# Kernel tuning notes

Measured on AMD Instinct MI355X. Metric: run time of the kernel, lower is better.

## Reference

```python
import jax, jax.numpy as jnp
import numpy as np

B, T, D, H = 4, 2048, 1024, 16
DK = D // H  # 64


def setup_inputs() -> dict:
    key = jax.random.key(0)
    ks = jax.random.split(key, 8)
    std = 1.0 / np.sqrt(2.0 * D)  # initialize_weights: normal(0, 1/sqrt(2*d_model*(i_layer+1))), i_layer=0
    inp = {
        "q": jax.random.normal(ks[0], (B, T, D), jnp.float32),
        "k": jax.random.normal(ks[1], (B, T, D), jnp.float32),
        "v": jax.random.normal(ks[2], (B, T, D), jnp.float32),
        "Wq": jax.random.normal(ks[3], (D, D), jnp.float32) * std,
        "Wk": jax.random.normal(ks[4], (D, D), jnp.float32) * std,
        "Wv": jax.random.normal(ks[5], (D, D), jnp.float32) * std,
        "Wo": jax.random.normal(ks[6], (D, D), jnp.float32) * std,
        "bq": jnp.zeros((D,), jnp.float32),
        "bk": jnp.zeros((D,), jnp.float32),
        "bv": jnp.zeros((D,), jnp.float32),
        "bo": jnp.zeros((D,), jnp.float32),
    }
    return inp


def _split_heads(x):
    # (B,T,D) -> (B,H,T,DK), same as x.view(B,T,H,DK).transpose(1,2)
    b, t, _ = x.shape
    return x.reshape(b, t, H, DK).transpose(0, 2, 1, 3)


def reference(q, k, v, Wq, Wk, Wv, Wo, bq, bk, bv, bo):
    # Linear projections (torch Linear: x @ W.T + b)
    qh = _split_heads(q @ Wq.T + bq)  # (B,H,T,DK)
    kh = _split_heads(k @ Wk.T + bk)
    vh = _split_heads(v @ Wv.T + bv)

    # scaled dot-product similarities: (B,H,Tq,Tk)
    scores = jnp.einsum("bhqd,bhkd->bhqk", qh, kh) / jnp.sqrt(jnp.float32(DK))

    # causal mask: tril(ones)==0 positions filled with -inf
    tq, tk = scores.shape[-2], scores.shape[-1]
    causal = jnp.tril(jnp.ones((tq, tk), dtype=bool))
    scores = jnp.where(causal, scores, jnp.float32(-jnp.inf))

    attn = jax.nn.softmax(scores, axis=-1)  # (B,H,Tq,Tk)
    ctx = jnp.einsum("bhqk,bhkd->bhqd", attn, vh)  # (B,H,Tq,DK)

    # merge heads: (B,H,T,DK) -> (B,T,D), then output projection
    merged = ctx.transpose(0, 2, 1, 3).reshape(q.shape[0], tq, D)
    return merged @ Wo.T + bo
```

## Files before the change

### kernel.cpp

```cpp
#include <hip/hip_runtime.h>
#include <hip/hip_bf16.h>
#include <stdint.h>

#define B_ 4
#define T_ 2048
#define D_ 1024
#define H_ 16
#define DK_ 64
#define M_ (B_*T_)

typedef __attribute__((ext_vector_type(8))) short bf16x8;
typedef __attribute__((ext_vector_type(4))) short bf16x4;
typedef __attribute__((ext_vector_type(4))) float f32x4;
typedef __hip_bfloat16 bf16;

__device__ __forceinline__ void gld_lds16(const bf16* g, bf16* l) {
  __builtin_amdgcn_global_load_lds((const __attribute__((address_space(1))) void*)g,
                                   (__attribute__((address_space(3))) void*)l,
                                   16, 0, 0);
}

__device__ __forceinline__ short bfbits(float f) {
  union { bf16 h; short s; } u; u.h = __float2bfloat16(f); return u.s;
}

__global__ __launch_bounds__(256) void cvt_all(
    const float* __restrict__ q, const float* __restrict__ k, const float* __restrict__ v,
    const float* __restrict__ wq, const float* __restrict__ wk,
    const float* __restrict__ wv, const float* __restrict__ wo,
    bf16* __restrict__ qb, bf16* __restrict__ kb, bf16* __restrict__ vb,
    bf16* __restrict__ wqb, bf16* __restrict__ wkb,
    bf16* __restrict__ wvb, bf16* __restrict__ wob) {
  int gid = blockIdx.x * 256 + threadIdx.x;
  const float* src; bf16* dst; int off;
  if (gid < 6291456) {
    int s = gid >> 21; off = gid & 2097151;
    src = (s == 0) ? q : (s == 1) ? k : v;
    dst = (s == 0) ? qb : (s == 1) ? kb : vb;
  } else {
    int g2 = gid - 6291456;
    int s = g2 >> 18; off = g2 & 262143;
    src = (s == 0) ? wq : (s == 1) ? wk : (s == 2) ? wv : wo;
    dst = (s == 0) ? wqb : (s == 1) ? wkb : (s == 2) ? wvb : wob;
  }
  float4 val = reinterpret_cast<const float4*>(src)[off];
  union { ushort4 u; bf16 h[4]; } o;
  o.h[0] = __float2bfloat16(val.x);
  o.h[1] = __float2bfloat16(val.y);
  o.h[2] = __float2bfloat16(val.z);
  o.h[3] = __float2bfloat16(val.w);
  reinterpret_cast<ushort4*>(dst)[off] = o.u;
}

__global__ __launch_bounds__(512) void proj_qkv(
    const bf16* __restrict__ qb, const bf16* __restrict__ kb, const bf16* __restrict__ vb,
    const bf16* __restrict__ Wqb, const bf16* __restrict__ Wkb, const bf16* __restrict__ Wvb,
    const float* __restrict__ bq, const float* __restrict__ bk, const float* __restrict__ bv,
    bf16* __restrict__ Qh, bf16* __restrict__ Kh, bf16* __restrict__ Vt) {
  constexpr int K = 1024;
  constexpr int BK = 64;
  __shared__ __align__(16) bf16 As[256 * BK];
  __shared__ __align__(16) bf16 Bs[128 * BK];

  const int z = blockIdx.z;
  const bool vt = (z == 2);
  const bf16* A  = (z == 0) ? qb : (z == 1) ? kb : Wvb;
  const bf16* Bm = (z == 0) ? Wqb : (z == 1) ? Wkb : vb;
  const float* bias = (z == 0) ? bq : (z == 1) ? bk : bv;
  bf16* out = (z == 0) ? Qh : (z == 1) ? Kh : Vt;
  const float scale = (z == 0) ? 0.125f * 1.4426950408889634f : 1.0f;

  const int bid = blockIdx.x + 32 * blockIdx.y;
  int bm, bn;
  if (vt) {
    bm = bid >> 6; bn = bid & 63;
  } else {
    const int xcd = bid & 7, loc = bid >> 3;
    bm = xcd * 4 + (loc & 3);
    bn = loc >> 2;
  }

  const int tid = threadIdx.x;
  const int w = tid >> 6, l = tid & 63;
  const int wm = w >> 1, wn = w & 1;
  const int lr = l & 15, lk = l >> 4;

  f32x4 acc[4][4] = {};

  for (int k0 = 0; k0 < K; k0 += BK) {
#pragma unroll
    for (int i = 0; i < 4; ++i) {
      int p = i * 512 + tid;
      int row = p >> 3;
      int so = (p & 7) ^ (row & 7);
      gld_lds16(A + (size_t)(bm * 256 + row) * K + k0 + so * 8, &As[p * 8]);
    }
#pragma unroll
    for (int i = 0; i < 2; ++i) {
      int p = i * 512 + tid;
      int row = p >> 3;
      int so = (p & 7) ^ (row & 7);
      gld_lds16(Bm + (size_t)(bn * 128 + row) * K + k0 + so * 8, &Bs[p * 8]);
    }
    __syncthreads();

#pragma unroll
    for (int kk = 0; kk < 2; ++kk) {
      bf16x8 af[4], bfr[4];
#pragma unroll
      for (int m = 0; m < 4; ++m) {
        int row = wm * 64 + m * 16 + lr;
        int slot = (kk * 4 + lk) ^ (row & 7);
        af[m] = *reinterpret_cast<const bf16x8*>(&As[row * BK + slot * 8]);
      }
#pragma unroll
      for (int n = 0; n < 4; ++n) {
        int row = wn * 64 + n * 16 + lr;
        int slot = (kk * 4 + lk) ^ (row & 7);
        bfr[n] = *reinterpret_cast<const bf16x8*>(&Bs[row * BK + slot * 8]);
      }
#pragma unroll
      for (int m = 0; m < 4; ++m)
#pragma unroll
        for (int n = 0; n < 4; ++n)
          acc[m][n] = __builtin_amdgcn_mfma_f32_16x16x32_bf16(af[m], bfr[n], acc[m][n], 0, 0, 0);
    }
    __syncthreads();
  }

  const int crow0 = bm * 256 + wm * 64;
  const int ccol0 = bn * 128 + wn * 64;
#pragma unroll
  for (int m = 0; m < 4; ++m) {
#pragma unroll
    for (int n = 0; n < 4; ++n) {
#pragma unroll
      for (int r = 0; r < 4; ++r) {
        const int row = crow0 + m * 16 + lk * 4 + r;
        const int col = ccol0 + n * 16 + lr;
        if (!vt) {
          float vv = (acc[m][n][r] + bias[col]) * scale;
          size_t idx = (((size_t)(row >> 11) * H_ + (col >> 6)) * T_ + (row & (T_ - 1))) * DK_ + (col & (DK_ - 1));
          out[idx] = __float2bfloat16(vv);
        } else {
          float vv = acc[m][n][r] + bias[row];
          size_t idx = (size_t)(col >> 11) * ((size_t)H_ * DK_ * T_) + (size_t)row * T_ + (col & (T_ - 1));
          out[idx] = __float2bfloat16(vv);
        }
      }
    }
  }
}

__global__ __launch_bounds__(512) void gemm_out(const bf16* __restrict__ A,
                                                const bf16* __restrict__ Bm,
                                                const float* __restrict__ bias,
                                                float* __restrict__ Cout) {
  constexpr int K = 1024;
  constexpr int BK = 64;
  __shared__ __align__(16) bf16 As[256 * BK];
  __shared__ __align__(16) bf16 Bs[128 * BK];

  const int bid = blockIdx.x + 32 * blockIdx.y;
  const int xcd = bid & 7, loc = bid >> 3;
  const int bm = xcd * 4 + (loc & 3);
  const int bn = loc >> 2;

  const int tid = threadIdx.x;
  const int w = tid >> 6, l = tid & 63;
  const int wm = w >> 1, wn = w & 1;
  const int lr = l & 15, lk = l >> 4;

  f32x4 acc[4][4] = {};

  for (int k0 = 0; k0 < K; k0 += BK) {
#pragma unroll
    for (int i = 0; i < 4; ++i) {
      int p = i * 512 + tid;
      int row = p >> 3;
      int so = (p & 7) ^ (row & 7);
      gld_lds16(A + (size_t)(bm * 256 + row) * K + k0 + so * 8, &As[p * 8]);
    }
#pragma unroll
    for (int i = 0; i < 2; ++i) {
      int p = i * 512 + tid;
      int row = p >> 3;
      int so = (p & 7) ^ (row & 7);
      gld_lds16(Bm + (size_t)(bn * 128 + row) * K + k0 + so * 8, &Bs[p * 8]);
    }
    __syncthreads();

#pragma unroll
    for (int kk = 0; kk < 2; ++kk) {
      bf16x8 af[4], bfr[4];
#pragma unroll
      for (int m = 0; m < 4; ++m) {
        int row = wm * 64 + m * 16 + lr;
        int slot = (kk * 4 + lk) ^ (row & 7);
        af[m] = *reinterpret_cast<const bf16x8*>(&As[row * BK + slot * 8]);
      }
#pragma unroll
      for (int n = 0; n < 4; ++n) {
        int row = wn * 64 + n * 16 + lr;
        int slot = (kk * 4 + lk) ^ (row & 7);
        bfr[n] = *reinterpret_cast<const bf16x8*>(&Bs[row * BK + slot * 8]);
      }
#pragma unroll
      for (int m = 0; m < 4; ++m)
#pragma unroll
        for (int n = 0; n < 4; ++n)
          acc[m][n] = __builtin_amdgcn_mfma_f32_16x16x32_bf16(af[m], bfr[n], acc[m][n], 0, 0, 0);
    }
    __syncthreads();
  }

  const int crow0 = bm * 256 + wm * 64;
  const int ccol0 = bn * 128 + wn * 64;
#pragma unroll
  for (int m = 0; m < 4; ++m) {
#pragma unroll
    for (int n = 0; n < 4; ++n) {
#pragma unroll
      for (int r = 0; r < 4; ++r) {
        const int row = crow0 + m * 16 + lk * 4 + r;
        const int col = ccol0 + n * 16 + lr;
        Cout[(size_t)row * D_ + col] = acc[m][n][r] + bias[col];
      }
    }
  }
}

__global__ __launch_bounds__(256, 7) void attn_fwd(const bf16* __restrict__ Qh,
                                                   const bf16* __restrict__ Kh,
                                                   const bf16* __restrict__ Vt,
                                                   bf16* __restrict__ ctx) {
  __shared__ __align__(16) bf16 Kbuf[2][32 * 64];
  __shared__ __align__(16) bf16 Vbuf[2][32 * 64];
  __shared__ __align__(16) char Ps[4][16 * 80];

  const int tid = threadIdx.x, w = tid >> 6, l = tid & 63;
  const int lr = l & 15, lk = l >> 4;
  const int bid = blockIdx.x;
  const int head = bid & 63;
  const int t = 31 - (bid >> 6);
  char* Pw = &Ps[w][0];

  const bf16* Qb = Qh + (size_t)head * T_ * DK_;
  const bf16* Kb = Kh + (size_t)head * T_ * DK_;
  const bf16* Vb = Vt + (size_t)head * DK_ * T_;
  const int bb = head >> 4, hh = head & 15;

  const int r0 = t * 64;
  const int nt32 = 2 * (t + 1);
  const int qrow = r0 + w * 16 + lr;
  const int jd = (r0 + w * 16) >> 5;

  const bf16* qp = Qb + (size_t)qrow * DK_ + lk * 8;
  bf16x8 qf0 = *reinterpret_cast<const bf16x8*>(qp);
  bf16x8 qf1 = *reinterpret_cast<const bf16x8*>(qp + 32);

  f32x4 oacc[4] = {};
  float srow = 0.f;

  {
    int p = tid;
    int krow = p >> 3;
    int kso = (p & 7) ^ (krow & 7);
    gld_lds16(Kb + (size_t)krow * DK_ + kso * 8, &Kbuf[0][p * 8]);
    int vrow = p >> 3;
    int u = (p & 7) ^ (vrow & 7);
    int dk = vrow * 2 + (u >> 2);
    gld_lds16(Vb + (size_t)dk * T_ + (u & 3) * 8, &Vbuf[0][p * 8]);
  }
  __syncthreads();

  int buf = 0;
#pragma unroll 1
  for (int j = 0; j < nt32; ++j) {
    if (j + 1 < nt32) {
      const int k0n = (j + 1) * 32;
      int p = tid;
      int krow = p >> 3;
      int kso = (p & 7) ^ (krow & 7);
      gld_lds16(Kb + (size_t)(k0n + krow) * DK_ + kso * 8, &Kbuf[buf ^ 1][p * 8]);
      int vrow = p >> 3;
      int u = (p & 7) ^ (vrow & 7);
      int dk = vrow * 2 + (u >> 2);
      gld_lds16(Vb + (size_t)dk * T_ + k0n + (u & 3) * 8, &Vbuf[buf ^ 1][p * 8]);
    }

    if (j <= jd) {
      f32x4 sacc[2] = {};
      __builtin_amdgcn_s_setprio(1);
#pragma unroll
      for (int n = 0; n < 2; ++n) {
        int row = n * 16 + lr;
        int s0 = lk ^ (row & 7);
        int s1 = (4 + lk) ^ (row & 7);
        bf16x8 kf0 = *reinterpret_cast<const bf16x8*>(&Kbuf[buf][row * 64 + s0 * 8]);
        bf16x8 kf1 = *reinterpret_cast<const bf16x8*>(&Kbuf[buf][row * 64 + s1 * 8]);
        sacc[n] = __builtin_amdgcn_mfma_f32_16x16x32_bf16(kf0, qf0, sacc[n], 0, 0, 0);
        sacc[n] = __builtin_amdgcn_mfma_f32_16x16x32_bf16(kf1, qf1, sacc[n], 0, 0, 0);
      }
      __builtin_amdgcn_s_setprio(0);

      if (j == jd) {
#pragma unroll
        for (int n = 0; n < 2; ++n)
#pragma unroll
          for (int r = 0; r < 4; ++r)
            if (j * 32 + n * 16 + lk * 4 + r > qrow) sacc[n][r] = -1e30f;
      }

      float ts = 0.f;
#pragma unroll
      for (int n = 0; n < 2; ++n) {
        float p0 = __builtin_exp2f(sacc[n][0]);
        float p1 = __builtin_exp2f(sacc[n][1]);
        float p2 = __builtin_exp2f(sacc[n][2]);
        float p3 = __builtin_exp2f(sacc[n][3]);
        ts += (p0 + p1) + (p2 + p3);
        bf16x4 pk;
        pk[0] = bfbits(p0); pk[1] = bfbits(p1); pk[2] = bfbits(p2); pk[3] = bfbits(p3);
        *reinterpret_cast<bf16x4*>(Pw + lr * 80 + n * 32 + lk * 8) = pk;
      }
      ts += __shfl_xor(ts, 16, 64);
      ts += __shfl_xor(ts, 32, 64);
      srow += ts;

      bf16x8 pa = *reinterpret_cast<const bf16x8*>(Pw + lr * 80 + lk * 16);

      __builtin_amdgcn_s_setprio(1);
#pragma unroll
      for (int n = 0; n < 4; ++n) {
        int rowp = n * 8 + (lr >> 1);
        int u = (lr & 1) * 4 + lk;
        int s = u ^ (rowp & 7);
        bf16x8 vf = *reinterpret_cast<const bf16x8*>(&Vbuf[buf][rowp * 64 + s * 8]);
        oacc[n] = __builtin_amdgcn_mfma_f32_16x16x32_bf16(vf, pa, oacc[n], 0, 0, 0);
      }
      __builtin_amdgcn_s_setprio(0);
    }

    __syncthreads();
    buf ^= 1;
  }

  const float inv = 1.0f / srow;
#pragma unroll
  for (int n = 0; n < 4; ++n) {
    bf16x4 pk;
#pragma unroll
    for (int r = 0; r < 4; ++r) pk[r] = bfbits(oacc[n][r] * inv);
    *reinterpret_cast<bf16x4*>(&ctx[((size_t)(bb * T_ + qrow)) * D_ + hh * DK_ + n * 16 + lk * 4]) = pk;
  }
}

extern "C" void kernel_launch(void* const* d_in, const int* in_sizes, int n_in,
                              void* d_out, int out_size, void* d_ws, size_t ws_size,
                              hipStream_t stream) {
  const float* q  = (const float*)d_in[0];
  const float* k  = (const float*)d_in[1];
  const float* v  = (const float*)d_in[2];
  const float* Wq = (const float*)d_in[3];
  const float* Wk = (const float*)d_in[4];
  const float* Wv = (const float*)d_in[5];
  const float* Wo = (const float*)d_in[6];
  const float* bq = (const float*)d_in[7];
  const float* bk = (const float*)d_in[8];
  const float* bv = (const float*)d_in[9];
  const float* bo = (const float*)d_in[10];

  constexpr size_t E_IN = (size_t)M_ * D_;
  constexpr size_t E_W  = (size_t)D_ * D_;
  char* ws = (char*)d_ws;
  size_t off = 0;
  bf16* qb  = (bf16*)(ws + off); off += E_IN * 2;
  bf16* kb  = (bf16*)(ws + off); off += E_IN * 2;
  bf16* vb  = (bf16*)(ws + off); off += E_IN * 2;
  bf16* Wqb = (bf16*)(ws + off); off += E_W * 2;
  bf16* Wkb = (bf16*)(ws + off); off += E_W * 2;
  bf16* Wvb = (bf16*)(ws + off); off += E_W * 2;
  bf16* Wob = (bf16*)(ws + off); off += E_W * 2;
  bf16* Qh  = (bf16*)(ws + off); off += E_IN * 2;
  bf16* Kh  = (bf16*)(ws + off); off += E_IN * 2;
  bf16* Vtw = (bf16*)(ws + off); off += E_IN * 2;
  bf16* ctx = (bf16*)(ws + off); off += E_IN * 2;

  cvt_all<<<dim3(28672), dim3(256), 0, stream>>>(q, k, v, Wq, Wk, Wv, Wo,
                                                 qb, kb, vb, Wqb, Wkb, Wvb, Wob);

  proj_qkv<<<dim3(32, 8, 3), dim3(512), 0, stream>>>(qb, kb, vb, Wqb, Wkb, Wvb,
                                                     bq, bk, bv, Qh, Kh, Vtw);

  attn_fwd<<<dim3(2048), dim3(256), 0, stream>>>(Qh, Kh, Vtw, ctx);

  gemm_out<<<dim3(32, 8), dim3(512), 0, stream>>>(ctx, Wob, bo, (float*)d_out);
}
```

Before: 191.6 us.

## Warp-specialize projection GEMMs with producer waves and double-buffered LDS

Both projection GEMM kernels now split the 8 waves into 4 producer waves, which issue global-to-LDS loads into a double buffer one k-tile ahead, and 4 consumer waves. Each consumer wave computes a 64x128 sub-tile with MFMA at raised scheduling priority. The aim is to overlap global memory loads with matrix math instead of serialising load, barrier and compute each k-step. In exchange, half the waves do no MFMA work, each compute wave holds twice the accumulators (more register pressure), and LDS use doubles, which may lower occupancy.

```diff
diff --git a/kernel.cpp b/kernel.cpp
--- a/kernel.cpp
+++ b/kernel.cpp
@@ -59,8 +59,9 @@
     bf16* __restrict__ Qh, bf16* __restrict__ Kh, bf16* __restrict__ Vt) {
   constexpr int K = 1024;
   constexpr int BK = 64;
-  __shared__ __align__(16) bf16 As[256 * BK];
-  __shared__ __align__(16) bf16 Bs[128 * BK];
+  constexpr int NT = 16;
+  __shared__ __align__(16) bf16 As[2][256 * 64];
+  __shared__ __align__(16) bf16 Bs[2][128 * 64];
 
   const int z = blockIdx.z;
   const bool vt = (z == 2);
@@ -82,70 +83,84 @@
 
   const int tid = threadIdx.x;
   const int w = tid >> 6, l = tid & 63;
-  const int wm = w >> 1, wn = w & 1;
   const int lr = l & 15, lk = l >> 4;
 
-  f32x4 acc[4][4] = {};
-
-  for (int k0 = 0; k0 < K; k0 += BK) {
-#pragma unroll
-    for (int i = 0; i < 4; ++i) {
-      int p = i * 512 + tid;
-      int row = p >> 3;
-      int so = (p & 7) ^ (row & 7);
-      gld_lds16(A + (size_t)(bm * 256 + row) * K + k0 + so * 8, &As[p * 8]);
-    }
-#pragma unroll
-    for (int i = 0; i < 2; ++i) {
-      int p = i * 512 + tid;
-      int row = p >> 3;
-      int so = (p & 7) ^ (row & 7);
-      gld_lds16(Bm + (size_t)(bn * 128 + row) * K + k0 + so * 8, &Bs[p * 8]);
-    }
+  if (w >= 4) {
+    const int pt = tid - 256;
+    auto stage = [&](int t, int b) {
+#pragma unroll
+      for (int i = 0; i < 8; ++i) {
+        int p = i * 256 + pt;
+        int row = p >> 3;
+        int so = (p & 7) ^ (row & 7);
+        gld_lds16(A + (size_t)(bm * 256 + row) * K + t * BK + so * 8, &As[b][p * 8]);
+      }
+#pragma unroll
+      for (int i = 0; i < 4; ++i) {
+        int p = i * 256 + pt;
+        int row = p >> 3;
+        int so = (p & 7) ^ (row & 7);
+        gld_lds16(Bm + (size_t)(bn * 128 + row) * K + t * BK + so * 8, &Bs[b][p * 8]);
+      }
+    };
+    stage(0, 0);
     __syncthreads();
-
-#pragma unroll
-    for (int kk = 0; kk < 2; ++kk) {
-      bf16x8 af[4], bfr[4];
-#pragma unroll
-      for (int m = 0; m < 4; ++m) {
-        int row = wm * 64 + m * 16 + lr;
-        int slot = (kk * 4 + lk) ^ (row & 7);
-        af[m] = *reinterpret_cast<const bf16x8*>(&As[row * BK + slot * 8]);
-      }
-#pragma unroll
-      for (int n = 0; n < 4; ++n) {
-        int row = wn * 64 + n * 16 + lr;
-        int slot = (kk * 4 + lk) ^ (row & 7);
-        bfr[n] = *reinterpret_cast<const bf16x8*>(&Bs[row * BK + slot * 8]);
-      }
-#pragma unroll
-      for (int m = 0; m < 4; ++m)
-#pragma unroll
-        for (int n = 0; n < 4; ++n)
-          acc[m][n] = __builtin_amdgcn_mfma_f32_16x16x32_bf16(af[m], bfr[n], acc[m][n], 0, 0, 0);
-    }
+#pragma unroll 1
+    for (int t = 0; t < NT; ++t) {
+      if (t + 1 < NT) stage(t + 1, (t + 1) & 1);
+      __syncthreads();
+    }
+  } else {
+    f32x4 acc[4][8] = {};
     __syncthreads();
-  }
-
-  const int crow0 = bm * 256 + wm * 64;
-  const int ccol0 = bn * 128 + wn * 64;
-#pragma unroll
-  for (int m = 0; m < 4; ++m) {
-#pragma unroll
-    for (int n = 0; n < 4; ++n) {
-#pragma unroll
-      for (int r = 0; r < 4; ++r) {
-        const int row = crow0 + m * 16 + lk * 4 + r;
-        const int col = ccol0 + n * 16 + lr;
-        if (!vt) {
-          float vv = (acc[m][n][r] + bias[col]) * scale;
-          size_t idx = (((size_t)(row >> 11) * H_ + (col >> 6)) * T_ + (row & (T_ - 1))) * DK_ + (col & (DK_ - 1));
-          out[idx] = __float2bfloat16(vv);
-        } else {
-          float vv = acc[m][n][r] + bias[row];
-          size_t idx = (size_t)(col >> 11) * ((size_t)H_ * DK_ * T_) + (size_t)row * T_ + (col & (T_ - 1));
-          out[idx] = __float2bfloat16(vv);
+#pragma unroll 1
+    for (int t = 0; t < NT; ++t) {
+      const int b = t & 1;
+#pragma unroll
+      for (int kk = 0; kk < 2; ++kk) {
+        bf16x8 af[4], bfr[8];
+#pragma unroll
+        for (int m = 0; m < 4; ++m) {
+          int row = w * 64 + m * 16 + lr;
+          int slot = (kk * 4 + lk) ^ (row & 7);
+          af[m] = *reinterpret_cast<const bf16x8*>(&As[b][row * 64 + slot * 8]);
+        }
+#pragma unroll
+        for (int n = 0; n < 8; ++n) {
+          int row = n * 16 + lr;
+          int slot = (kk * 4 + lk) ^ (row & 7);
+          bfr[n] = *reinterpret_cast<const bf16x8*>(&Bs[b][row * 64 + slot * 8]);
+        }
+        __builtin_amdgcn_s_setprio(1);
+#pragma unroll
+        for (int m = 0; m < 4; ++m)
+#pragma unroll
+          for (int n = 0; n < 8; ++n)
+            acc[m][n] = __builtin_amdgcn_mfma_f32_16x16x32_bf16(af[m], bfr[n], acc[m][n], 0, 0, 0);
+        __builtin_amdgcn_s_setprio(0);
+      }
+      __syncthreads();
+    }
+
+    const int crow0 = bm * 256 + w * 64;
+    const int ccol0 = bn * 128;
+#pragma unroll
+    for (int m = 0; m < 4; ++m) {
+#pragma unroll
+      for (int n = 0; n < 8; ++n) {
+#pragma unroll
+        for (int r = 0; r < 4; ++r) {
+          const int row = crow0 + m * 16 + lk * 4 + r;
+          const int col = ccol0 + n * 16 + lr;
+          if (!vt) {
+            float vv = (acc[m][n][r] + bias[col]) * scale;
+            size_t idx = (((size_t)(row >> 11) * H_ + (col >> 6)) * T_ + (row & (T_ - 1))) * DK_ + (col & (DK_ - 1));
+            out[idx] = __float2bfloat16(vv);
+          } else {
+            float vv = acc[m][n][r] + bias[row];
+            size_t idx = (size_t)(col >> 11) * ((size_t)H_ * DK_ * T_) + (size_t)row * T_ + (col & (T_ - 1));
+            out[idx] = __float2bfloat16(vv);
+          }
         }
       }
     }
@@ -158,8 +173,9 @@
                                                 float* __restrict__ Cout) {
   constexpr int K = 1024;
   constexpr int BK = 64;
-  __shared__ __align__(16) bf16 As[256 * BK];
-  __shared__ __align__(16) bf16 Bs[128 * BK];
+  constexpr int NT = 16;
+  __shared__ __align__(16) bf16 As[2][256 * 64];
+  __shared__ __align__(16) bf16 Bs[2][128 * 64];
 
   const int bid = blockIdx.x + 32 * blockIdx.y;
   const int xcd = bid & 7, loc = bid >> 3;
@@ -168,63 +184,77 @@
 
   const int tid = threadIdx.x;
   const int w = tid >> 6, l = tid & 63;
-  const int wm = w >> 1, wn = w & 1;
   const int lr = l & 15, lk = l >> 4;
 
-  f32x4 acc[4][4] = {};
-
-  for (int k0 = 0; k0 < K; k0 += BK) {
-#pragma unroll
-    for (int i = 0; i < 4; ++i) {
-      int p = i * 512 + tid;
-      int row = p >> 3;
-      int so = (p & 7) ^ (row & 7);
-      gld_lds16(A + (size_t)(bm * 256 + row) * K + k0 + so * 8, &As[p * 8]);
-    }
-#pragma unroll
-    for (int i = 0; i < 2; ++i) {
-      int p = i * 512 + tid;
-      int row = p >> 3;
-      int so = (p & 7) ^ (row & 7);
-      gld_lds16(Bm + (size_t)(bn * 128 + row) * K + k0 + so * 8, &Bs[p * 8]);
-    }
+  if (w >= 4) {
+    const int pt = tid - 256;
+    auto stage = [&](int t, int b) {
+#pragma unroll
+      for (int i = 0; i < 8; ++i) {
+        int p = i * 256 + pt;
+        int row = p >> 3;
+        int so = (p & 7) ^ (row & 7);
+        gld_lds16(A + (size_t)(bm * 256 + row) * K + t * BK + so * 8, &As[b][p * 8]);
+      }
+#pragma unroll
+      for (int i = 0; i < 4; ++i) {
+        int p = i * 256 + pt;
+        int row = p >> 3;
+        int so = (p & 7) ^ (row & 7);
+        gld_lds16(Bm + (size_t)(bn * 128 + row) * K + t * BK + so * 8, &Bs[b][p * 8]);
+      }
+    };
+    stage(0, 0);
     __syncthreads();
-
-#pragma unroll
-    for (int kk = 0; kk < 2; ++kk) {
-      bf16x8 af[4], bfr[4];
-#pragma unroll
-      for (int m = 0; m < 4; ++m) {
-        int row = wm * 64 + m * 16 + lr;
-        int slot = (kk * 4 + lk) ^ (row & 7);
-        af[m] = *reinterpret_cast<const bf16x8*>(&As[row * BK + slot * 8]);
-      }
-#pragma unroll
-      for (int n = 0; n < 4; ++n) {
-        int row = wn * 64 + n * 16 + lr;
-        int slot = (kk * 4 + lk) ^ (row & 7);
-        bfr[n] = *reinterpret_cast<const bf16x8*>(&Bs[row * BK + slot * 8]);
-      }
-#pragma unroll
-      for (int m = 0; m < 4; ++m)
-#pragma unroll
-        for (int n = 0; n < 4; ++n)
-          acc[m][n] = __builtin_amdgcn_mfma_f32_16x16x32_bf16(af[m], bfr[n], acc[m][n], 0, 0, 0);
-    }
+#pragma unroll 1
+    for (int t = 0; t < NT; ++t) {
+      if (t + 1 < NT) stage(t + 1, (t + 1) & 1);
+      __syncthreads();
+    }
+  } else {
+    f32x4 acc[4][8] = {};
     __syncthreads();
-  }
-
-  const int crow0 = bm * 256 + wm * 64;
-  const int ccol0 = bn * 128 + wn * 64;
-#pragma unroll
-  for (int m = 0; m < 4; ++m) {
-#pragma unroll
-    for (int n = 0; n < 4; ++n) {
-#pragma unroll
-      for (int r = 0; r < 4; ++r) {
-        const int row = crow0 + m * 16 + lk * 4 + r;
-        const int col = ccol0 + n * 16 + lr;
-        Cout[(size_t)row * D_ + col] = acc[m][n][r] + bias[col];
+#pragma unroll 1
+    for (int t = 0; t < NT; ++t) {
+      const int b = t & 1;
+#pragma unroll
+      for (int kk = 0; kk < 2; ++kk) {
+        bf16x8 af[4], bfr[8];
+#pragma unroll
+        for (int m = 0; m < 4; ++m) {
+          int row = w * 64 + m * 16 + lr;
+          int slot = (kk * 4 + lk) ^ (row & 7);
+          af[m] = *reinterpret_cast<const bf16x8*>(&As[b][row * 64 + slot * 8]);
+        }
+#pragma unroll
+        for (int n = 0; n < 8; ++n) {
+          int row = n * 16 + lr;
+          int slot = (kk * 4 + lk) ^ (row & 7);
+          bfr[n] = *reinterpret_cast<const bf16x8*>(&Bs[b][row * 64 + slot * 8]);
+        }
+        __builtin_amdgcn_s_setprio(1);
+#pragma unroll
+        for (int m = 0; m < 4; ++m)
+#pragma unroll
+          for (int n = 0; n < 8; ++n)
+            acc[m][n] = __builtin_amdgcn_mfma_f32_16x16x32_bf16(af[m], bfr[n], acc[m][n], 0, 0, 0);
+        __builtin_amdgcn_s_setprio(0);
+      }
+      __syncthreads();
+    }
+
+    const int crow0 = bm * 256 + w * 64;
+    const int ccol0 = bn * 128;
+#pragma unroll
+    for (int m = 0; m < 4; ++m) {
+#pragma unroll
+      for (int n = 0; n < 8; ++n) {
+#pragma unroll
+        for (int r = 0; r < 4; ++r) {
+          const int row = crow0 + m * 16 + lk * 4 + r;
+          const int col = ccol0 + n * 16 + lr;
+          Cout[(size_t)row * D_ + col] = acc[m][n][r] + bias[col];
+        }
       }
     }
   }
```

New measurement: 211.9 us. 10.6% more time.

## Fuse fp32-to-bf16 activation conversion into QKV projection GEMM

Applied to the files above, without the earlier changes.

Removes the separate conversion pass over the q/k/v activations. The projection kernel now loads fp32 activations straight into LDS with a swizzled layout and converts them to bf16 on the fly, which also saves the bf16 activation round trip through global memory. All three projections now compute the transposed product (W times x^T) with a uniform block mapping, and Q/K outputs are written as packed 4-element stores. Trade-offs: LDS use per block doubles for the B tile, each B-fragment read does per-element conversion work, and MFMA sections get raised wave priority.

```diff
diff --git a/kernel.cpp b/kernel.cpp
--- a/kernel.cpp
+++ b/kernel.cpp
@@ -19,30 +19,25 @@
                                    (__attribute__((address_space(3))) void*)l,
                                    16, 0, 0);
 }
+__device__ __forceinline__ void gld_lds16f(const float* g, float* l) {
+  __builtin_amdgcn_global_load_lds((const __attribute__((address_space(1))) void*)g,
+                                   (__attribute__((address_space(3))) void*)l,
+                                   16, 0, 0);
+}
 
 __device__ __forceinline__ short bfbits(float f) {
   union { bf16 h; short s; } u; u.h = __float2bfloat16(f); return u.s;
 }
 
-__global__ __launch_bounds__(256) void cvt_all(
-    const float* __restrict__ q, const float* __restrict__ k, const float* __restrict__ v,
+__global__ __launch_bounds__(256) void cvt_w(
     const float* __restrict__ wq, const float* __restrict__ wk,
     const float* __restrict__ wv, const float* __restrict__ wo,
-    bf16* __restrict__ qb, bf16* __restrict__ kb, bf16* __restrict__ vb,
     bf16* __restrict__ wqb, bf16* __restrict__ wkb,
     bf16* __restrict__ wvb, bf16* __restrict__ wob) {
   int gid = blockIdx.x * 256 + threadIdx.x;
-  const float* src; bf16* dst; int off;
-  if (gid < 6291456) {
-    int s = gid >> 21; off = gid & 2097151;
-    src = (s == 0) ? q : (s == 1) ? k : v;
-    dst = (s == 0) ? qb : (s == 1) ? kb : vb;
-  } else {
-    int g2 = gid - 6291456;
-    int s = g2 >> 18; off = g2 & 262143;
-    src = (s == 0) ? wq : (s == 1) ? wk : (s == 2) ? wv : wo;
-    dst = (s == 0) ? wqb : (s == 1) ? wkb : (s == 2) ? wvb : wob;
-  }
+  int s = gid >> 18, off = gid & 262143;
+  const float* src = (s == 0) ? wq : (s == 1) ? wk : (s == 2) ? wv : wo;
+  bf16* dst = (s == 0) ? wqb : (s == 1) ? wkb : (s == 2) ? wvb : wob;
   float4 val = reinterpret_cast<const float4*>(src)[off];
   union { ushort4 u; bf16 h[4]; } o;
   o.h[0] = __float2bfloat16(val.x);
@@ -53,32 +48,25 @@
 }
 
 __global__ __launch_bounds__(512) void proj_qkv(
-    const bf16* __restrict__ qb, const bf16* __restrict__ kb, const bf16* __restrict__ vb,
+    const float* __restrict__ qf, const float* __restrict__ kf, const float* __restrict__ vf,
     const bf16* __restrict__ Wqb, const bf16* __restrict__ Wkb, const bf16* __restrict__ Wvb,
     const float* __restrict__ bq, const float* __restrict__ bk, const float* __restrict__ bv,
     bf16* __restrict__ Qh, bf16* __restrict__ Kh, bf16* __restrict__ Vt) {
   constexpr int K = 1024;
   constexpr int BK = 64;
-  __shared__ __align__(16) bf16 As[256 * BK];
-  __shared__ __align__(16) bf16 Bs[128 * BK];
+  __shared__ __align__(16) bf16  As[256 * 64];
+  __shared__ __align__(16) float Bsf[128 * 64];
 
   const int z = blockIdx.z;
-  const bool vt = (z == 2);
-  const bf16* A  = (z == 0) ? qb : (z == 1) ? kb : Wvb;
-  const bf16* Bm = (z == 0) ? Wqb : (z == 1) ? Wkb : vb;
+  const bf16*  A  = (z == 0) ? Wqb : (z == 1) ? Wkb : Wvb;
+  const float* Bf = (z == 0) ? qf : (z == 1) ? kf : vf;
   const float* bias = (z == 0) ? bq : (z == 1) ? bk : bv;
   bf16* out = (z == 0) ? Qh : (z == 1) ? Kh : Vt;
   const float scale = (z == 0) ? 0.125f * 1.4426950408889634f : 1.0f;
 
   const int bid = blockIdx.x + 32 * blockIdx.y;
-  int bm, bn;
-  if (vt) {
-    bm = bid >> 6; bn = bid & 63;
-  } else {
-    const int xcd = bid & 7, loc = bid >> 3;
-    bm = xcd * 4 + (loc & 3);
-    bn = loc >> 2;
-  }
+  const int bm = bid >> 6;
+  const int bn = bid & 63;
 
   const int tid = threadIdx.x;
   const int w = tid >> 6, l = tid & 63;
@@ -96,11 +84,11 @@
       gld_lds16(A + (size_t)(bm * 256 + row) * K + k0 + so * 8, &As[p * 8]);
     }
 #pragma unroll
-    for (int i = 0; i < 2; ++i) {
+    for (int i = 0; i < 4; ++i) {
       int p = i * 512 + tid;
-      int row = p >> 3;
-      int so = (p & 7) ^ (row & 7);
-      gld_lds16(Bm + (size_t)(bn * 128 + row) * K + k0 + so * 8, &Bs[p * 8]);
+      int row = p >> 4;
+      int sc = (p & 15) ^ (row & 15);
+      gld_lds16f(Bf + (size_t)(bn * 128 + row) * K + k0 + sc * 4, &Bsf[p * 4]);
     }
     __syncthreads();
 
@@ -111,38 +99,60 @@
       for (int m = 0; m < 4; ++m) {
         int row = wm * 64 + m * 16 + lr;
         int slot = (kk * 4 + lk) ^ (row & 7);
-        af[m] = *reinterpret_cast<const bf16x8*>(&As[row * BK + slot * 8]);
+        af[m] = *reinterpret_cast<const bf16x8*>(&As[row * 64 + slot * 8]);
       }
 #pragma unroll
       for (int n = 0; n < 4; ++n) {
-        int row = wn * 64 + n * 16 + lr;
-        int slot = (kk * 4 + lk) ^ (row & 7);
-        bfr[n] = *reinterpret_cast<const bf16x8*>(&Bs[row * BK + slot * 8]);
-      }
+        int trow = wn * 64 + n * 16 + lr;
+        int c0 = kk * 8 + lk * 2;
+        int s0 = c0 ^ (trow & 15);
+        int s1 = (c0 + 1) ^ (trow & 15);
+        f32x4 lo = *reinterpret_cast<const f32x4*>(&Bsf[trow * 64 + s0 * 4]);
+        f32x4 hi = *reinterpret_cast<const f32x4*>(&Bsf[trow * 64 + s1 * 4]);
+        bf16x8 bb;
+        bb[0] = bfbits(lo[0]); bb[1] = bfbits(lo[1]);
+        bb[2] = bfbits(lo[2]); bb[3] = bfbits(lo[3]);
+        bb[4] = bfbits(hi[0]); bb[5] = bfbits(hi[1]);
+        bb[6] = bfbits(hi[2]); bb[7] = bfbits(hi[3]);
+        bfr[n] = bb;
+      }
+      __builtin_amdgcn_s_setprio(1);
 #pragma unroll
       for (int m = 0; m < 4; ++m)
 #pragma unroll
         for (int n = 0; n < 4; ++n)
           acc[m][n] = __builtin_amdgcn_mfma_f32_16x16x32_bf16(af[m], bfr[n], acc[m][n], 0, 0, 0);
+      __builtin_amdgcn_s_setprio(0);
     }
     __syncthreads();
   }
 
   const int crow0 = bm * 256 + wm * 64;
   const int ccol0 = bn * 128 + wn * 64;
-#pragma unroll
-  for (int m = 0; m < 4; ++m) {
-#pragma unroll
-    for (int n = 0; n < 4; ++n) {
-#pragma unroll
-      for (int r = 0; r < 4; ++r) {
-        const int row = crow0 + m * 16 + lk * 4 + r;
+  if (z < 2) {
+#pragma unroll
+    for (int m = 0; m < 4; ++m) {
+#pragma unroll
+      for (int n = 0; n < 4; ++n) {
+        const int row0 = crow0 + m * 16 + lk * 4;
         const int col = ccol0 + n * 16 + lr;
-        if (!vt) {
-          float vv = (acc[m][n][r] + bias[col]) * scale;
-          size_t idx = (((size_t)(row >> 11) * H_ + (col >> 6)) * T_ + (row & (T_ - 1))) * DK_ + (col & (DK_ - 1));
-          out[idx] = __float2bfloat16(vv);
-        } else {
+        bf16x4 pk;
+#pragma unroll
+        for (int r = 0; r < 4; ++r)
+          pk[r] = bfbits((acc[m][n][r] + bias[row0 + r]) * scale);
+        size_t idx = (((size_t)(col >> 11) * H_ + (row0 >> 6)) * T_ + (col & (T_ - 1))) * DK_ + (row0 & 63);
+        *reinterpret_cast<bf16x4*>(&out[idx]) = pk;
+      }
+    }
+  } else {
+#pragma unroll
+    for (int m = 0; m < 4; ++m) {
+#pragma unroll
+      for (int n = 0; n < 4; ++n) {
+#pragma unroll
+        for (int r = 0; r < 4; ++r) {
+          const int row = crow0 + m * 16 + lk * 4 + r;
+          const int col = ccol0 + n * 16 + lr;
           float vv = acc[m][n][r] + bias[row];
           size_t idx = (size_t)(col >> 11) * ((size_t)H_ * DK_ * T_) + (size_t)row * T_ + (col & (T_ - 1));
           out[idx] = __float2bfloat16(vv);
@@ -375,9 +385,6 @@
   constexpr size_t E_W  = (size_t)D_ * D_;
   char* ws = (char*)d_ws;
   size_t off = 0;
-  bf16* qb  = (bf16*)(ws + off); off += E_IN * 2;
-  bf16* kb  = (bf16*)(ws + off); off += E_IN * 2;
-  bf16* vb  = (bf16*)(ws + off); off += E_IN * 2;
   bf16* Wqb = (bf16*)(ws + off); off += E_W * 2;
   bf16* Wkb = (bf16*)(ws + off); off += E_W * 2;
   bf16* Wvb = (bf16*)(ws + off); off += E_W * 2;
@@ -387,10 +394,9 @@
   bf16* Vtw = (bf16*)(ws + off); off += E_IN * 2;
   bf16* ctx = (bf16*)(ws + off); off += E_IN * 2;
 
-  cvt_all<<<dim3(28672), dim3(256), 0, stream>>>(q, k, v, Wq, Wk, Wv, Wo,
-                                                 qb, kb, vb, Wqb, Wkb, Wvb, Wob);
-
-  proj_qkv<<<dim3(32, 8, 3), dim3(512), 0, stream>>>(qb, kb, vb, Wqb, Wkb, Wvb,
+  cvt_w<<<dim3(4096), dim3(256), 0, stream>>>(Wq, Wk, Wv, Wo, Wqb, Wkb, Wvb, Wob);
+
+  proj_qkv<<<dim3(32, 8, 3), dim3(512), 0, stream>>>(q, k, v, Wqb, Wkb, Wvb,
                                                      bq, bk, bv, Qh, Kh, Vtw);
 
   attn_fwd<<<dim3(2048), dim3(256), 0, stream>>>(Qh, Kh, Vtw, ctx);
```

Result: no change. 188.7 us (-1.5%).
